# Optimization experiments

Hardware: AMD Instinct MI355X
Metric: run time of the kernel (lower is better)

The kernel has to match this reference:

```python
import jax, jax.numpy as jnp
import numpy as np

B, C, H, W = 8, 64, 256, 256   # input images
FH, FW = 64, 64                # low-res feature map
S = 256                        # superpixels per image (num[i] == S)


def setup_inputs() -> dict:
    key = jax.random.key(0)
    k1, k2, k3 = jax.random.split(key, 3)
    inp = jax.random.normal(k1, (B, C, H, W), dtype=jnp.float32)
    feat = jax.random.normal(k2, (B, C, FH, FW), dtype=jnp.float32)
    sp = jax.random.randint(k3, (B, 1, H, W), 0, S).astype(jnp.int64)
    num = jnp.full((B,), S, dtype=jnp.int64)
    return {"input": inp, "feature": feat, "sp": sp, "num": num}


def bilinear_align_corners(x, out_h, out_w):
    # F.interpolate(x, size, mode='bilinear', align_corners=True)
    _, _, in_h, in_w = x.shape
    ys = jnp.linspace(0.0, in_h - 1.0, out_h)
    xs = jnp.linspace(0.0, in_w - 1.0, out_w)
    y0 = jnp.floor(ys).astype(jnp.int32)
    x0 = jnp.floor(xs).astype(jnp.int32)
    y1 = jnp.minimum(y0 + 1, in_h - 1)
    x1 = jnp.minimum(x0 + 1, in_w - 1)
    wy = (ys - y0.astype(ys.dtype)).reshape(1, 1, out_h, 1)
    wx = (xs - x0.astype(xs.dtype)).reshape(1, 1, 1, out_w)
    rows = x[:, :, y0, :] * (1.0 - wy) + x[:, :, y1, :] * wy   # [B,C,out_h,in_w]
    return rows[:, :, :, x0] * (1.0 - wx) + rows[:, :, :, x1] * wx


def segment_scalar_means(x, sp, num):
    # torch: mean_values[i][j] = mean(x[i][sp[i]==j]) over channels AND pixels
    b = x.shape[0]
    px = x.mean(axis=1).reshape(b, -1)           # channel-mean per pixel [B, HW]
    ids = sp.reshape(b, -1)                      # [B, HW]
    seg_sum = jax.vmap(lambda v, i: jax.ops.segment_sum(v, i, num_segments=S))(px, ids)
    seg_cnt = jax.vmap(lambda i: jax.ops.segment_sum(jnp.ones(i.shape, jnp.float32), i, num_segments=S))(ids)
    m = jnp.where(seg_cnt > 0, seg_sum / jnp.maximum(seg_cnt, 1.0), 0.0)  # nan_to_num(0)
    valid = jnp.arange(S)[None, :] < num[:, None]                          # j < num[i]
    return jnp.where(valid, m, 0.0)              # [B, S]


def similarity_matrix(m):
    # mean_values broadcast to [B,S,C] => 1 - ||diff||/sqrt(C) == 1 - |m_j - m_k|
    return 1.0 - jnp.abs(m[:, :, None] - m[:, None, :])   # [B, S, S]


def reference(input, feature, sp, num):
    feat = bilinear_align_corners(feature, input.shape[-1], input.shape[-1])
    mat1 = similarity_matrix(segment_scalar_means(input, sp, num))
    mat2 = similarity_matrix(segment_scalar_means(feat, sp, num))
    return jnp.mean(jnp.abs(mat1 - mat2))   # nn.L1Loss()
```

## Files before the change

kernel.cpp:

```cpp
#include <hip/hip_runtime.h>

#define NB 8
#define NC 64
#define NH 256
#define NW 256
#define HW (NH*NW)
#define NFH 64
#define NFW 64
#define FHW (NFH*NFW)
#define NS 256
#define PPA 2048
#define NPA (HW/PPA)
#define PPB 1024
#define NPB (HW/PPB)
#define NG 4
#define CPG (NC/NG)
#define NMAIN (NB*NPA*NG)
#define NRB (NB*NPB)

typedef float f32x4 __attribute__((ext_vector_type(4)));

__global__ __launch_bounds__(256) void
main_k(const float* __restrict__ input,
       const float* __restrict__ feature,
       const int* __restrict__ sp,
       float* __restrict__ part1,
       float* __restrict__ part2,
       float* __restrict__ partc,
       unsigned* __restrict__ counter) {
  __shared__ float s_bins[NS];
  __shared__ float s_fb[NS];
  __shared__ unsigned s_cnt[NS];
  __shared__ float s_frow[3][NFW];

  const int bid = blockIdx.x;
  const int tid = threadIdx.x;
  if (bid == 0 && tid == 0) *counter = 0u;

  if (bid < NMAIN) {
    const int g  = bid & (NG - 1);
    const int pb = (bid >> 2) & (NPA - 1);
    const int b  = bid >> 7;

    s_bins[tid] = 0.f;
    __syncthreads();

    const int base = pb * PPA;
    const float* ib = input + (size_t)(b * NC + g * CPG) * HW + base;
    const int o = tid * 4;
    f32x4 accA = (f32x4)(0.f);
    f32x4 accB = (f32x4)(0.f);
    #pragma unroll
    for (int c = 0; c < CPG; ++c) {
      accA += *reinterpret_cast<const f32x4*>(ib + (size_t)c * HW + o);
      accB += *reinterpret_cast<const f32x4*>(ib + (size_t)c * HW + 1024 + o);
    }
    const int4 idvA = *reinterpret_cast<const int4*>(sp + (size_t)b * HW + base + o);
    const int4 idvB = *reinterpret_cast<const int4*>(sp + (size_t)b * HW + base + 1024 + o);
    const float s = 1.0f / NC;
    atomicAdd(&s_bins[idvA.x], accA.x * s);
    atomicAdd(&s_bins[idvA.y], accA.y * s);
    atomicAdd(&s_bins[idvA.z], accA.z * s);
    atomicAdd(&s_bins[idvA.w], accA.w * s);
    atomicAdd(&s_bins[idvB.x], accB.x * s);
    atomicAdd(&s_bins[idvB.y], accB.y * s);
    atomicAdd(&s_bins[idvB.z], accB.z * s);
    atomicAdd(&s_bins[idvB.w], accB.w * s);
    __syncthreads();

    part1[(size_t)bid * NS + tid] = s_bins[tid];
  } else {
    const int r  = bid - NMAIN;
    const int b  = r >> 6;
    const int pb = r & (NPB - 1);

    const int h0    = pb * 4;
    const int y0min = (h0 * (NFH - 1)) / (NH - 1);

    s_fb[tid] = 0.f;
    s_cnt[tid] = 0u;
    if (tid < 192) s_frow[tid >> 6][tid & 63] = 0.f;
    __syncthreads();

    {
      const int px = tid & 63;
      const int q  = tid >> 6;
      const int r0 = min(y0min,     NFH - 1);
      const int r1 = min(y0min + 1, NFH - 1);
      const int r2 = min(y0min + 2, NFH - 1);
      const float* fb = feature + (size_t)(b * NC + q * 16) * FHW;
      float a0 = 0.f, a1 = 0.f, a2 = 0.f;
      #pragma unroll
      for (int c = 0; c < 16; ++c) {
        const float* fc = fb + (size_t)c * FHW;
        a0 += fc[r0 * NFW + px];
        a1 += fc[r1 * NFW + px];
        a2 += fc[r2 * NFW + px];
      }
      const float sc = 1.0f / NC;
      atomicAdd(&s_frow[0][px], a0 * sc);
      atomicAdd(&s_frow[1][px], a1 * sc);
      atomicAdd(&s_frow[2][px], a2 * sc);
    }
    __syncthreads();

    const int p0 = pb * PPB + tid * 4;
    const int4 idv = *reinterpret_cast<const int4*>(sp + (size_t)b * HW + p0);
    const int ids[4] = {idv.x, idv.y, idv.z, idv.w};

    const int h = p0 >> 8;
    const float yd = (float)h * (63.0f / 255.0f);
    const int y0 = (int)yd;
    const float wy = yd - (float)y0;
    const int y1 = min(y0 + 1, NFH - 1);
    const float* row0 = s_frow[y0 - y0min];
    const float* row1 = s_frow[y1 - y0min];

    #pragma unroll
    for (int i = 0; i < 4; ++i) {
      const int w = (p0 & 255) + i;
      const float xd = (float)w * (63.0f / 255.0f);
      const int x0 = (int)xd;
      const float wx = xd - (float)x0;
      const int x1 = min(x0 + 1, NFW - 1);
      float v0 = row0[x0] * (1.f - wy) + row1[x0] * wy;
      float v1 = row0[x1] * (1.f - wy) + row1[x1] * wy;
      float fv = v0 * (1.f - wx) + v1 * wx;
      atomicAdd(&s_fb[ids[i]], fv);
      atomicAdd(&s_cnt[ids[i]], 1u);
    }
    __syncthreads();

    part2[(size_t)r * NS + tid] = s_fb[tid];
    partc[(size_t)r * NS + tid] = (float)s_cnt[tid];
  }
}

__global__ __launch_bounds__(256) void
finalize_k(const float* __restrict__ part1,
           const float* __restrict__ part2,
           const float* __restrict__ partc,
           const int* __restrict__ num,
           float* __restrict__ partial,
           unsigned* __restrict__ counter,
           float* __restrict__ out) {
  __shared__ float m1[NS];
  __shared__ float m2[NS];
  __shared__ float red[256];
  const int b = blockIdx.x;
  const int j = threadIdx.x;

  float s1 = 0.f;
  const float* p1 = part1 + (size_t)b * (NMAIN / NB) * NS + j;
  #pragma unroll 8
  for (int t = 0; t < NMAIN / NB; ++t) s1 += p1[(size_t)t * NS];

  float s2 = 0.f, c = 0.f;
  const float* p2 = part2 + (size_t)b * 64 * NS + j;
  const float* pc = partc + (size_t)b * 64 * NS + j;
  #pragma unroll 8
  for (int t = 0; t < 64; ++t) { s2 += p2[(size_t)t * NS]; c += pc[(size_t)t * NS]; }

  const int nb = num[b];
  float v1 = 0.f, v2 = 0.f;
  if (j < nb && c > 0.f) {
    float invc = 1.0f / c;
    v1 = s1 * invc;
    v2 = s2 * invc;
  }
  m1[j] = v1; m2[j] = v2;
  __syncthreads();

  float accum = 0.f;
  #pragma unroll 8
  for (int k = 0; k < NS; ++k) {
    accum += fabsf(fabsf(v1 - m1[k]) - fabsf(v2 - m2[k]));
  }
  red[j] = accum;
  __syncthreads();
  for (int st = 128; st > 0; st >>= 1) {
    if (j < st) red[j] += red[j + st];
    __syncthreads();
  }

  if (j == 0) {
    atomicExch(&partial[b], red[0]);
    __threadfence();
    unsigned old = atomicAdd(counter, 1u);
    if (old == NB - 1) {
      __threadfence();
      float sAll = 0.f;
      #pragma unroll
      for (int i = 0; i < NB; ++i) sAll += atomicAdd(&partial[i], 0.0f);
      out[0] = sAll / (float)(NB * NS * NS);
      *counter = 0u;
    }
  }
}

extern "C" void kernel_launch(void* const* d_in, const int* in_sizes, int n_in,
                              void* d_out, int out_size, void* d_ws, size_t ws_size,
                              hipStream_t stream) {
  const float* input   = (const float*)d_in[0];
  const float* feature = (const float*)d_in[1];
  const int*   sp      = (const int*)d_in[2];
  const int*   num     = (const int*)d_in[3];
  float* out = (float*)d_out;

  float* ws      = (float*)d_ws;
  float*    part1   = ws;
  float*    part2   = part1 + (size_t)NMAIN * NS;
  float*    partc   = part2 + (size_t)NRB * NS;
  float*    partial = partc + (size_t)NRB * NS;
  unsigned* counter = (unsigned*)(partial + 8);

  main_k<<<NMAIN + NRB, 256, 0, stream>>>(input, feature, sp, part1, part2, partc, counter);
  finalize_k<<<NB, 256, 0, stream>>>(part1, part2, partc, num, partial, counter, out);
}
```

Baseline: 53.08 us.

## Replace per-block partial buffers with global atomic accumulation into per-image sums

```diff
diff --git a/kernel.cpp b/kernel.cpp
--- a/kernel.cpp
+++ b/kernel.cpp
@@ -20,14 +20,17 @@
 
 typedef float f32x4 __attribute__((ext_vector_type(4)));
 
+__global__ __launch_bounds__(256) void zero_k(float* __restrict__ acc ) {
+  for (int i = threadIdx.x; i < 3 * NB * NS + 9; i += 256) acc[i] = 0.f;
+}
+
 __global__ __launch_bounds__(256) void
 main_k(const float* __restrict__ input,
        const float* __restrict__ feature,
        const int* __restrict__ sp,
-       float* __restrict__ part1,
-       float* __restrict__ part2,
-       float* __restrict__ partc,
-       unsigned* __restrict__ counter) {
+       float* __restrict__ sum1,
+       float* __restrict__ sum2,
+       float* __restrict__ cntf) {
   __shared__ float s_bins[NS];
   __shared__ float s_fb[NS];
   __shared__ unsigned s_cnt[NS];
@@ -35,7 +38,6 @@
 
   const int bid = blockIdx.x;
   const int tid = threadIdx.x;
-  if (bid == 0 && tid == 0) *counter = 0u;
 
   if (bid < NMAIN) {
     const int g  = bid & (NG - 1);
@@ -52,11 +54,13 @@
     f32x4 accB = (f32x4)(0.f);
     #pragma unroll
     for (int c = 0; c < CPG; ++c) {
-      accA += *reinterpret_cast<const f32x4*>(ib + (size_t)c * HW + o);
-      accB += *reinterpret_cast<const f32x4*>(ib + (size_t)c * HW + 1024 + o);
-    }
-    const int4 idvA = *reinterpret_cast<const int4*>(sp + (size_t)b * HW + base + o);
-    const int4 idvB = *reinterpret_cast<const int4*>(sp + (size_t)b * HW + base + 1024 + o);
+      const float* p = ib + (size_t)c * HW + o;
+      accA += *reinterpret_cast<const f32x4*>(p);
+      accB += *reinterpret_cast<const f32x4*>(p + 1024);
+    }
+    const int* spb = sp + (size_t)b * HW + base + o;
+    const int4 idvA = *reinterpret_cast<const int4*>(spb);
+    const int4 idvB = *reinterpret_cast<const int4*>(spb + 1024);
     const float s = 1.0f / NC;
     atomicAdd(&s_bins[idvA.x], accA.x * s);
     atomicAdd(&s_bins[idvA.y], accA.y * s);
@@ -68,7 +72,7 @@
     atomicAdd(&s_bins[idvB.w], accB.w * s);
     __syncthreads();
 
-    part1[(size_t)bid * NS + tid] = s_bins[tid];
+    atomicAdd(&sum1[b * NS + tid], s_bins[tid]);
   } else {
     const int r  = bid - NMAIN;
     const int b  = r >> 6;
@@ -131,15 +135,15 @@
     }
     __syncthreads();
 
-    part2[(size_t)r * NS + tid] = s_fb[tid];
-    partc[(size_t)r * NS + tid] = (float)s_cnt[tid];
+    atomicAdd(&sum2[b * NS + tid], s_fb[tid]);
+    atomicAdd(&cntf[b * NS + tid], (float)s_cnt[tid]);
   }
 }
 
 __global__ __launch_bounds__(256) void
-finalize_k(const float* __restrict__ part1,
-           const float* __restrict__ part2,
-           const float* __restrict__ partc,
+finalize_k(const float* __restrict__ sum1,
+           const float* __restrict__ sum2,
+           const float* __restrict__ cntf,
            const int* __restrict__ num,
            float* __restrict__ partial,
            unsigned* __restrict__ counter,
@@ -150,16 +154,9 @@
   const int b = blockIdx.x;
   const int j = threadIdx.x;
 
-  float s1 = 0.f;
-  const float* p1 = part1 + (size_t)b * (NMAIN / NB) * NS + j;
-  #pragma unroll 8
-  for (int t = 0; t < NMAIN / NB; ++t) s1 += p1[(size_t)t * NS];
-
-  float s2 = 0.f, c = 0.f;
-  const float* p2 = part2 + (size_t)b * 64 * NS + j;
-  const float* pc = partc + (size_t)b * 64 * NS + j;
-  #pragma unroll 8
-  for (int t = 0; t < 64; ++t) { s2 += p2[(size_t)t * NS]; c += pc[(size_t)t * NS]; }
+  const float s1 = sum1[b * NS + j];
+  const float s2 = sum2[b * NS + j];
+  const float c  = cntf[b * NS + j];
 
   const int nb = num[b];
   float v1 = 0.f, v2 = 0.f;
@@ -193,7 +190,6 @@
       #pragma unroll
       for (int i = 0; i < NB; ++i) sAll += atomicAdd(&partial[i], 0.0f);
       out[0] = sAll / (float)(NB * NS * NS);
-      *counter = 0u;
     }
   }
 }
@@ -207,13 +203,14 @@
   const int*   num     = (const int*)d_in[3];
   float* out = (float*)d_out;
 
-  float* ws      = (float*)d_ws;
-  float*    part1   = ws;
-  float*    part2   = part1 + (size_t)NMAIN * NS;
-  float*    partc   = part2 + (size_t)NRB * NS;
-  float*    partial = partc + (size_t)NRB * NS;
+  float* ws = (float*)d_ws;
+  float*    sum1    = ws;
+  float*    sum2    = ws + NB * NS;
+  float*    cntf    = ws + 2 * NB * NS;
+  float*    partial = ws + 3 * NB * NS;
   unsigned* counter = (unsigned*)(partial + 8);
 
-  main_k<<<NMAIN + NRB, 256, 0, stream>>>(input, feature, sp, part1, part2, partc, counter);
-  finalize_k<<<NB, 256, 0, stream>>>(part1, part2, partc, num, partial, counter, out);
-}
+  zero_k<<<1, 256, 0, stream>>>(ws);
+  main_k<<<NMAIN + NRB, 256, 0, stream>>>(input, feature, sp, sum1, sum2, cntf);
+  finalize_k<<<NB, 256, 0, stream>>>(sum1, sum2, cntf, num, partial, counter, out);
+}
```

Result: no change. 53.86 us (+1.5%).
